# Optimization experiments

Hardware: AMD Instinct MI355X
Metric: run time of the kernel (lower is better)

The kernel has to match this reference:

```python
import jax, jax.numpy as jnp
import numpy as np

B, N_PEP, N_REC, EMB, OUT = 4, 4096, 10, 256, 256


def setup_inputs() -> dict:
    key = jax.random.key(0)
    ks = jax.random.split(key, 9)
    s_emb = 1.0 / np.sqrt(EMB)
    s_2emb = 1.0 / np.sqrt(2 * EMB)
    return {
        "rec_node_feat": jax.random.normal(ks[0], (B, N_PEP, N_REC, EMB), jnp.float32),
        "pep_node_feat": jax.random.normal(ks[1], (B, N_PEP, EMB), jnp.float32),
        "edge_feat": jax.random.normal(ks[2], (B, N_PEP, N_REC, EMB), jnp.float32),
        "Wp_w": jax.random.uniform(ks[3], (OUT, EMB), jnp.float32, -s_emb, s_emb),
        "Wp_b": jax.random.uniform(ks[4], (OUT,), jnp.float32, -s_emb, s_emb),
        "Wr_w": jax.random.uniform(ks[5], (OUT, 2 * EMB), jnp.float32, -s_2emb, s_2emb),
        "Wr_b": jax.random.uniform(ks[6], (OUT,), jnp.float32, -s_2emb, s_2emb),
        "Wv_w": jax.random.uniform(ks[7], (OUT, 2 * EMB), jnp.float32, -s_2emb, s_2emb),
        "Wv_b": jax.random.uniform(ks[8], (OUT,), jnp.float32, -s_2emb, s_2emb),
    }


def reference(rec_node_feat, pep_node_feat, edge_feat,
              Wp_w, Wp_b, Wr_w, Wr_b, Wv_w, Wv_b):
    # pep query: [B, N_pep, out]
    pep_query = jnp.einsum('bnd,od->bno', pep_node_feat, Wp_w) + Wp_b
    # receptor + edge concat: [B, N_pep, 10, 2*emb]
    rec_edge = jnp.concatenate((rec_node_feat, edge_feat), axis=3)
    value = jnp.einsum('bnrd,od->bnro', rec_edge, Wv_w) + Wv_b  # [B,N,10,out]
    key_ = jnp.einsum('bnrd,od->bnro', rec_edge, Wr_w) + Wr_b   # [B,N,10,out]
    scale = 1.0 / np.sqrt(OUT).astype(np.float32)
    # elementwise QK dot over out dim -> [B, N, 10]
    logits = jnp.einsum('bno,bnro->bnr', pep_query, key_) * scale
    attention = jax.nn.softmax(logits, axis=2)  # softmax over 10 neighbors
    # weighted value sum + residual projection
    out = pep_query + jnp.einsum('bnr,bnro->bno', attention, value)
    return out
```

## Files before the change

kernel.cpp:

```cpp
#include <hip/hip_runtime.h>
#include <hip/hip_bf16.h>

#define N_TOK   16384
#define NREC    10
#define EMB     256
#define TWO_EMB 512
#define OUTD    256
#define T_BLK   16
#define THREADS 512

typedef __bf16 bf16x8 __attribute__((ext_vector_type(8)));
typedef float  f32x4  __attribute__((ext_vector_type(4)));

static __device__ __forceinline__ unsigned int f2bf_bits(float f) {
    unsigned int u = __builtin_bit_cast(unsigned int, f);
    u = (u + 0x7fffu + ((u >> 16) & 1u)) >> 16;
    return u & 0xffffu;
}
static __device__ __forceinline__ unsigned int pack2(float a, float b) {
    return f2bf_bits(a) | (f2bf_bits(b) << 16);
}
static __device__ __forceinline__ float bflo(unsigned int u) {
    return __builtin_bit_cast(float, u << 16);
}
static __device__ __forceinline__ float bfhi(unsigned int u) {
    return __builtin_bit_cast(float, u & 0xffff0000u);
}

__global__ void prep_wfrag(const float* __restrict__ Wp,
                           const float* __restrict__ Wr,
                           const float* __restrict__ Wv,
                           short* __restrict__ wp_frag,
                           short* __restrict__ wr_frag,
                           short* __restrict__ wv_frag) {
    int idx = blockIdx.x * blockDim.x + threadIdx.x;
    if (idx < 16 * 8 * 64 * 8) {
        int j = idx & 7, lane = (idx >> 3) & 63, kt = (idx >> 9) & 7, nt = idx >> 12;
        int n = nt * 16 + (lane & 15), k = kt * 32 + ((lane >> 4) << 3) + j;
        wp_frag[idx] = (short)f2bf_bits(Wp[n * EMB + k]);
    }
    if (idx < 32 * 8 * 64 * 8) {
        int j = idx & 7, lane = (idx >> 3) & 63, kt = (idx >> 9) & 7, nt = idx >> 12;
        int n = nt * 16 + (lane & 15), k = kt * 32 + ((lane >> 4) << 3) + j;
        wr_frag[idx] = (short)f2bf_bits(Wr[k * TWO_EMB + n]);
    }
    if (idx < 16 * 16 * 64 * 8) {
        int j = idx & 7, lane = (idx >> 3) & 63, kt = (idx >> 9) & 15, nt = idx >> 13;
        int n = nt * 16 + (lane & 15), k = kt * 32 + ((lane >> 4) << 3) + j;
        wv_frag[idx] = (short)f2bf_bits(Wv[n * TWO_EMB + k]);
    }
}

template<int USE_FRAG>
static __device__ __forceinline__ bf16x8 load_b_rm(const short* __restrict__ frag,
                                                   const float* __restrict__ W,
                                                   int n, int k, int ld) {
    if constexpr (USE_FRAG) {
        return *reinterpret_cast<const bf16x8*>(frag);
    } else {
        const float* s = W + (long)n * ld + k;
        float4 f0 = *reinterpret_cast<const float4*>(s);
        float4 f1 = *reinterpret_cast<const float4*>(s + 4);
        uint4 t = { pack2(f0.x, f0.y), pack2(f0.z, f0.w), pack2(f1.x, f1.y), pack2(f1.z, f1.w) };
        return __builtin_bit_cast(bf16x8, t);
    }
}
template<int USE_FRAG>
static __device__ __forceinline__ bf16x8 load_b_tr(const short* __restrict__ frag,
                                                   const float* __restrict__ W,
                                                   int n, int k, int ld) {
    if constexpr (USE_FRAG) {
        return *reinterpret_cast<const bf16x8*>(frag);
    } else {
        unsigned int p[4];
        #pragma unroll
        for (int jj = 0; jj < 4; ++jj)
            p[jj] = pack2(W[(long)(k + 2 * jj) * ld + n], W[(long)(k + 2 * jj + 1) * ld + n]);
        uint4 t = { p[0], p[1], p[2], p[3] };
        return __builtin_bit_cast(bf16x8, t);
    }
}

static __device__ __forceinline__ void stream_token(
    const float* __restrict__ bp,
    const unsigned char* __restrict__ qrb,
    unsigned char* __restrict__ xz,
    int t, int lane,
    float4 s0l, float4 s0h, float4 s1l, float4 s1h,
    float4 s2l, float4 s2h, float4 s3l, float4 s3h)
{
    uint4 qw = *reinterpret_cast<const uint4*>(qrb + t * 1024 + lane * 16);
    const float qa0 = bflo(qw.x), qa1 = bfhi(qw.x), qa2 = bflo(qw.y), qa3 = bfhi(qw.y);
    const float qa4 = bflo(qw.z), qa5 = bfhi(qw.z), qa6 = bflo(qw.w), qa7 = bfhi(qw.w);
    const float C = 0.0625f * 1.4426950408889634f;

    float s = 0.f;
    float4 xb0 = make_float4(0.f, 0.f, 0.f, 0.f), xb1 = xb0;

    #define LD(r, sl, sh) { sl = *reinterpret_cast<const float4*>(bp + (r) * EMB); \
                            sh = *reinterpret_cast<const float4*>(bp + (r) * EMB + 4); }
    #define PROC(sl, sh) { \
        float p = qa0*(sl).x + qa1*(sl).y + qa2*(sl).z + qa3*(sl).w \
                + qa4*(sh).x + qa5*(sh).y + qa6*(sh).z + qa7*(sh).w; \
        p += __shfl_xor(p, 1); \
        p += __shfl_xor(p, 2); \
        p += __shfl_xor(p, 4); \
        p += __shfl_xor(p, 8); \
        p += __shfl_xor(p, 16); \
        p += __shfl_xor(p, 32); \
        float e = exp2f(p * C);                       \
        s += e; \
        xb0.x += e*(sl).x; xb0.y += e*(sl).y; xb0.z += e*(sl).z; xb0.w += e*(sl).w; \
        xb1.x += e*(sh).x; xb1.y += e*(sh).y; xb1.z += e*(sh).z; xb1.w += e*(sh).w; }

    PROC(s0l, s0h); LD(4, s0l, s0h);
    PROC(s1l, s1h); LD(5, s1l, s1h);
    PROC(s2l, s2h); LD(6, s2l, s2h);
    PROC(s3l, s3h); LD(7, s3l, s3h);
    PROC(s0l, s0h); LD(8, s0l, s0h);
    PROC(s1l, s1h); LD(9, s1l, s1h);
    PROC(s2l, s2h);
    PROC(s3l, s3h);
    PROC(s0l, s0h);
    PROC(s1l, s1h);
    #undef LD
    #undef PROC

    const float inv = 1.f / s;
    uint4 wv4 = { pack2(xb0.x * inv, xb0.y * inv), pack2(xb0.z * inv, xb0.w * inv),
                  pack2(xb1.x * inv, xb1.y * inv), pack2(xb1.z * inv, xb1.w * inv) };
    *reinterpret_cast<uint4*>(xz + 1024 * t + ((lane * 16) ^ ((t & 7) << 4))) = wv4;
}

template<int USE_FRAG>
__launch_bounds__(THREADS, 4)
__global__ void ga5_fused(const float* __restrict__ rec,
                          const float* __restrict__ pep,
                          const float* __restrict__ edge,
                          const float* __restrict__ Wp_w,
                          const float* __restrict__ Wp_b,
                          const float* __restrict__ Wr_w,
                          const float* __restrict__ Wv_w,
                          const float* __restrict__ Wv_b,
                          const short* __restrict__ wp_frag,
                          const short* __restrict__ wr_frag,
                          const short* __restrict__ wv_frag,
                          float* __restrict__ out) {
    __shared__ __align__(16) unsigned char xz[T_BLK * 1024];
    __shared__ __align__(16) unsigned char qbf[T_BLK * 512];
    __shared__ __align__(16) unsigned char qrb[T_BLK * 1024];

    const int tid  = threadIdx.x;
    const int lane = tid & 63;
    const int wave = tid >> 6;
    const int tok0 = blockIdx.x * T_BLK;

    #pragma unroll
    for (int it = 0; it < 2; ++it) {
        int idx = tid + it * THREADS;
        int row = idx >> 6, d4 = (idx & 63) << 2;
        float4 f = *reinterpret_cast<const float4*>(pep + (long)(tok0 + row) * EMB + d4);
        uint2 w = { pack2(f.x, f.y), pack2(f.z, f.w) };
        *reinterpret_cast<uint2*>(xz + 512 * row + ((d4 * 2) ^ ((row & 7) << 4))) = w;
    }
    __syncthreads();

    {
        f32x4 qacc[2] = {};
        #pragma unroll
        for (int kt = 0; kt < 8; ++kt) {
            int kk = kt * 32 + ((lane >> 4) << 3);
            int row = lane & 15;
            bf16x8 a = *reinterpret_cast<const bf16x8*>(xz + 512 * row + ((kk * 2) ^ ((row & 7) << 4)));
            #pragma unroll
            for (int ntl = 0; ntl < 2; ++ntl) {
                int nt = wave * 2 + ntl;
                bf16x8 b = load_b_rm<USE_FRAG>(wp_frag + ((nt * 8 + kt) * 64 + lane) * 8,
                                               Wp_w, nt * 16 + (lane & 15), kk, EMB);
                qacc[ntl] = __builtin_amdgcn_mfma_f32_16x16x32_bf16(a, b, qacc[ntl], 0, 0, 0);
            }
        }
        #pragma unroll
        for (int ntl = 0; ntl < 2; ++ntl) {
            int n = (wave * 2 + ntl) * 16 + (lane & 15);
            float bias = Wp_b[n];
            #pragma unroll
            for (int i = 0; i < 4; ++i) {
                int row = ((lane >> 4) << 2) + i;
                float v = qacc[ntl][i] + bias;
                *reinterpret_cast<unsigned short*>(qbf + 512 * row + ((n * 2) ^ ((row & 7) << 4)))
                    = (unsigned short)f2bf_bits(v);
            }
        }
    }

    const float* srcA = (lane < 32) ? rec : edge;
    const int dloc = (lane * 8) & 255;
    const float* baseA = srcA + (long)(tok0 + wave * 2) * NREC * EMB + dloc;
    const float* baseB = baseA + (long)NREC * EMB;
    float4 a0l = *reinterpret_cast<const float4*>(baseA + 0 * EMB);
    float4 a0h = *reinterpret_cast<const float4*>(baseA + 0 * EMB + 4);
    float4 a1l = *reinterpret_cast<const float4*>(baseA + 1 * EMB);
    float4 a1h = *reinterpret_cast<const float4*>(baseA + 1 * EMB + 4);
    float4 a2l = *reinterpret_cast<const float4*>(baseA + 2 * EMB);
    float4 a2h = *reinterpret_cast<const float4*>(baseA + 2 * EMB + 4);
    float4 a3l = *reinterpret_cast<const float4*>(baseA + 3 * EMB);
    float4 a3h = *reinterpret_cast<const float4*>(baseA + 3 * EMB + 4);
    __syncthreads();

    {
        f32x4 racc[4] = {};
        #pragma unroll
        for (int kt = 0; kt < 8; ++kt) {
            int kk = kt * 32 + ((lane >> 4) << 3);
            int row = lane & 15;
            bf16x8 a = *reinterpret_cast<const bf16x8*>(qbf + 512 * row + ((kk * 2) ^ ((row & 7) << 4)));
            #pragma unroll
            for (int ntl = 0; ntl < 4; ++ntl) {
                int nt = wave * 4 + ntl;
                bf16x8 b = load_b_tr<USE_FRAG>(wr_frag + ((nt * 8 + kt) * 64 + lane) * 8,
                                               Wr_w, nt * 16 + (lane & 15), kk, TWO_EMB);
                racc[ntl] = __builtin_amdgcn_mfma_f32_16x16x32_bf16(a, b, racc[ntl], 0, 0, 0);
            }
        }
        #pragma unroll
        for (int ntl = 0; ntl < 4; ++ntl) {
            int n = (wave * 4 + ntl) * 16 + (lane & 15);
            #pragma unroll
            for (int i = 0; i < 4; ++i) {
                int row = ((lane >> 4) << 2) + i;
                *reinterpret_cast<unsigned short*>(qrb + row * 1024 + n * 2)
                    = (unsigned short)f2bf_bits(racc[ntl][i]);
            }
        }
    }
    __syncthreads();

    stream_token(baseA, qrb, xz, wave * 2, lane, a0l, a0h, a1l, a1h, a2l, a2h, a3l, a3h);
    {
        float4 b0l = *reinterpret_cast<const float4*>(baseB + 0 * EMB);
        float4 b0h = *reinterpret_cast<const float4*>(baseB + 0 * EMB + 4);
        float4 b1l = *reinterpret_cast<const float4*>(baseB + 1 * EMB);
        float4 b1h = *reinterpret_cast<const float4*>(baseB + 1 * EMB + 4);
        float4 b2l = *reinterpret_cast<const float4*>(baseB + 2 * EMB);
        float4 b2h = *reinterpret_cast<const float4*>(baseB + 2 * EMB + 4);
        float4 b3l = *reinterpret_cast<const float4*>(baseB + 3 * EMB);
        float4 b3h = *reinterpret_cast<const float4*>(baseB + 3 * EMB + 4);
        stream_token(baseB, qrb, xz, wave * 2 + 1, lane, b0l, b0h, b1l, b1h, b2l, b2h, b3l, b3h);
    }
    __syncthreads();

    {
        f32x4 oacc[2] = {};
        #pragma unroll
        for (int kt = 0; kt < 16; ++kt) {
            int kk = kt * 32 + ((lane >> 4) << 3);
            int row = lane & 15;
            bf16x8 a = *reinterpret_cast<const bf16x8*>(xz + 1024 * row + ((kk * 2) ^ ((row & 7) << 4)));
            #pragma unroll
            for (int ntl = 0; ntl < 2; ++ntl) {
                int nt = wave * 2 + ntl;
                bf16x8 b = load_b_rm<USE_FRAG>(wv_frag + ((nt * 16 + kt) * 64 + lane) * 8,
                                               Wv_w, nt * 16 + (lane & 15), kk, TWO_EMB);
                oacc[ntl] = __builtin_amdgcn_mfma_f32_16x16x32_bf16(a, b, oacc[ntl], 0, 0, 0);
            }
        }
        #pragma unroll
        for (int ntl = 0; ntl < 2; ++ntl) {
            int n = (wave * 2 + ntl) * 16 + (lane & 15);
            float bv = Wv_b[n];
            #pragma unroll
            for (int i = 0; i < 4; ++i) {
                int row = ((lane >> 4) << 2) + i;
                unsigned short qu = *reinterpret_cast<const unsigned short*>(
                    qbf + 512 * row + ((n * 2) ^ ((row & 7) << 4)));
                float qv = __builtin_bit_cast(float, (unsigned int)qu << 16);
                out[(long)(tok0 + row) * OUTD + n] = qv + oacc[ntl][i] + bv;
            }
        }
    }
}

extern "C" void kernel_launch(void* const* d_in, const int* in_sizes, int n_in,
                              void* d_out, int out_size, void* d_ws, size_t ws_size,
                              hipStream_t stream) {
    const float* rec  = (const float*)d_in[0];
    const float* pep  = (const float*)d_in[1];
    const float* edge = (const float*)d_in[2];
    const float* Wp_w = (const float*)d_in[3];
    const float* Wp_b = (const float*)d_in[4];
    const float* Wr_w = (const float*)d_in[5];
    const float* Wv_w = (const float*)d_in[7];
    const float* Wv_b = (const float*)d_in[8];
    float* out = (float*)d_out;

    const size_t wp_elems = 16 * 8 * 64 * 8;
    const size_t wr_elems = 32 * 8 * 64 * 8;
    const size_t wv_elems = 16 * 16 * 64 * 8;
    const size_t need = (wp_elems + wr_elems + wv_elems) * sizeof(short);
    short* wp_frag = (short*)d_ws;
    short* wr_frag = wp_frag + wp_elems;
    short* wv_frag = wr_frag + wr_elems;

    if (ws_size >= need) {
        prep_wfrag<<<512, 256, 0, stream>>>(Wp_w, Wr_w, Wv_w, wp_frag, wr_frag, wv_frag);
        ga5_fused<1><<<N_TOK / T_BLK, THREADS, 0, stream>>>(rec, pep, edge, Wp_w, Wp_b, Wr_w,
                                                            Wv_w, Wv_b, wp_frag, wr_frag, wv_frag, out);
    } else {
        ga5_fused<0><<<N_TOK / T_BLK, THREADS, 0, stream>>>(rec, pep, edge, Wp_w, Wp_b, Wr_w,
                                                            Wv_w, Wv_b, wp_frag, wr_frag, wv_frag, out);
    }
}
```

Baseline: 97.53 us.

## Split fused kernel into query, streaming and output-projection kernels

Splits the single fused kernel into three launches. The first computes the bf16 query and the query-key projection and writes them to workspace and the output buffer. The second streams rec/edge with one wave per token, computing softmax and the weighted sum into the output buffer as scratch. The third runs the Wv GEMM and adds the residual. The goal is to decouple the memory-bound streaming phase from the GEMM phases so occupancy is higher, and the cross-lane reduction moves to DPP. The cost is extra launches and global round trips for intermediates, plus in-place reuse of the output buffer.

Result: slower. 152.0 us (+55.8%).

```diff
diff --git a/kernel.cpp b/kernel.cpp
--- a/kernel.cpp
+++ b/kernel.cpp
@@ -6,8 +6,6 @@
 #define EMB     256
 #define TWO_EMB 512
 #define OUTD    256
-#define T_BLK   16
-#define THREADS 512
 
 typedef __bf16 bf16x8 __attribute__((ext_vector_type(8)));
 typedef float  f32x4  __attribute__((ext_vector_type(4)));
@@ -25,6 +23,24 @@
 }
 static __device__ __forceinline__ float bfhi(unsigned int u) {
     return __builtin_bit_cast(float, u & 0xffff0000u);
+}
+static __device__ __forceinline__ bf16x8 pack8(float4 f0, float4 f1) {
+    uint4 t = { pack2(f0.x, f0.y), pack2(f0.z, f0.w), pack2(f1.x, f1.y), pack2(f1.z, f1.w) };
+    return __builtin_bit_cast(bf16x8, t);
+}
+
+static __device__ __forceinline__ float wave_sum(float p) {
+    p += __builtin_bit_cast(float, __builtin_amdgcn_update_dpp(
+             0, __builtin_bit_cast(int, p), 0x121, 0xf, 0xf, true));
+    p += __builtin_bit_cast(float, __builtin_amdgcn_update_dpp(
+             0, __builtin_bit_cast(int, p), 0x122, 0xf, 0xf, true));
+    p += __builtin_bit_cast(float, __builtin_amdgcn_update_dpp(
+             0, __builtin_bit_cast(int, p), 0x124, 0xf, 0xf, true));
+    p += __builtin_bit_cast(float, __builtin_amdgcn_update_dpp(
+             0, __builtin_bit_cast(int, p), 0x128, 0xf, 0xf, true));
+    p += __shfl_xor(p, 16);
+    p += __shfl_xor(p, 32);
+    return p;
 }
 
 __global__ void prep_wfrag(const float* __restrict__ Wp,
@@ -59,10 +75,8 @@
         return *reinterpret_cast<const bf16x8*>(frag);
     } else {
         const float* s = W + (long)n * ld + k;
-        float4 f0 = *reinterpret_cast<const float4*>(s);
-        float4 f1 = *reinterpret_cast<const float4*>(s + 4);
-        uint4 t = { pack2(f0.x, f0.y), pack2(f0.z, f0.w), pack2(f1.x, f1.y), pack2(f1.z, f1.w) };
-        return __builtin_bit_cast(bf16x8, t);
+        return pack8(*reinterpret_cast<const float4*>(s),
+                     *reinterpret_cast<const float4*>(s + 4));
     }
 }
 template<int USE_FRAG>
@@ -81,18 +95,109 @@
     }
 }
 
-static __device__ __forceinline__ void stream_token(
-    const float* __restrict__ bp,
-    const unsigned char* __restrict__ qrb,
-    unsigned char* __restrict__ xz,
-    int t, int lane,
-    float4 s0l, float4 s0h, float4 s1l, float4 s1h,
-    float4 s2l, float4 s2h, float4 s3l, float4 s3h)
-{
-    uint4 qw = *reinterpret_cast<const uint4*>(qrb + t * 1024 + lane * 16);
+template<int USE_FRAG>
+__launch_bounds__(256, 4)
+__global__ void ga_qr(const float* __restrict__ pep,
+                      const float* __restrict__ Wp_w,
+                      const float* __restrict__ Wp_b,
+                      const float* __restrict__ Wr_w,
+                      const short* __restrict__ wp_frag,
+                      const short* __restrict__ wr_frag,
+                      unsigned short* __restrict__ qws,
+                      unsigned short* __restrict__ qrws) {
+    __shared__ __align__(16) unsigned char qbf[16 * 512];
+
+    const int tid  = threadIdx.x;
+    const int lane = tid & 63;
+    const int wave = tid >> 6;
+    const int tok0 = blockIdx.x * 16;
+
+    #pragma unroll
+    for (int pass = 0; pass < 2; ++pass) {
+        f32x4 qacc[2] = {};
+        #pragma unroll
+        for (int kt = 0; kt < 8; ++kt) {
+            int kk = kt * 32 + ((lane >> 4) << 3);
+            int row = lane & 15;
+            const float* s = pep + (long)(tok0 + row) * EMB + kk;
+            bf16x8 a = pack8(*reinterpret_cast<const float4*>(s),
+                             *reinterpret_cast<const float4*>(s + 4));
+            #pragma unroll
+            for (int ntl = 0; ntl < 2; ++ntl) {
+                int nt = wave * 4 + pass * 2 + ntl;
+                bf16x8 b = load_b_rm<USE_FRAG>(wp_frag + ((nt * 8 + kt) * 64 + lane) * 8,
+                                               Wp_w, nt * 16 + (lane & 15), kk, EMB);
+                qacc[ntl] = __builtin_amdgcn_mfma_f32_16x16x32_bf16(a, b, qacc[ntl], 0, 0, 0);
+            }
+        }
+        #pragma unroll
+        for (int ntl = 0; ntl < 2; ++ntl) {
+            int n = (wave * 4 + pass * 2 + ntl) * 16 + (lane & 15);
+            float bias = Wp_b[n];
+            #pragma unroll
+            for (int i = 0; i < 4; ++i) {
+                int row = ((lane >> 4) << 2) + i;
+                unsigned short u = (unsigned short)f2bf_bits(qacc[ntl][i] + bias);
+                *reinterpret_cast<unsigned short*>(qbf + 512 * row + ((n * 2) ^ ((row & 7) << 4))) = u;
+                qws[(long)(tok0 + row) * OUTD + n] = u;
+            }
+        }
+    }
+    __syncthreads();
+
+    #pragma unroll
+    for (int pass = 0; pass < 4; ++pass) {
+        f32x4 racc[2] = {};
+        #pragma unroll
+        for (int kt = 0; kt < 8; ++kt) {
+            int kk = kt * 32 + ((lane >> 4) << 3);
+            int row = lane & 15;
+            bf16x8 a = *reinterpret_cast<const bf16x8*>(qbf + 512 * row + ((kk * 2) ^ ((row & 7) << 4)));
+            #pragma unroll
+            for (int ntl = 0; ntl < 2; ++ntl) {
+                int nt = wave * 8 + pass * 2 + ntl;
+                bf16x8 b = load_b_tr<USE_FRAG>(wr_frag + ((nt * 8 + kt) * 64 + lane) * 8,
+                                               Wr_w, nt * 16 + (lane & 15), kk, TWO_EMB);
+                racc[ntl] = __builtin_amdgcn_mfma_f32_16x16x32_bf16(a, b, racc[ntl], 0, 0, 0);
+            }
+        }
+        #pragma unroll
+        for (int ntl = 0; ntl < 2; ++ntl) {
+            int n = (wave * 8 + pass * 2 + ntl) * 16 + (lane & 15);
+            #pragma unroll
+            for (int i = 0; i < 4; ++i) {
+                int row = ((lane >> 4) << 2) + i;
+                qrws[(long)(tok0 + row) * TWO_EMB + n] = (unsigned short)f2bf_bits(racc[ntl][i]);
+            }
+        }
+    }
+}
+
+__launch_bounds__(256, 8)
+__global__ void ga_stream(const float* __restrict__ rec,
+                          const float* __restrict__ edge,
+                          unsigned short* qr_xbar) {
+    const int lane = threadIdx.x & 63;
+    const int wave = threadIdx.x >> 6;
+    const int t = blockIdx.x * 4 + wave;
+
+    const float* srcA = (lane < 32) ? rec : edge;
+    const int dloc = (lane * 8) & 255;
+    const float* bp = srcA + (long)t * NREC * EMB + dloc;
+
+    uint4 qw = *reinterpret_cast<const uint4*>(qr_xbar + (long)t * TWO_EMB + lane * 8);
     const float qa0 = bflo(qw.x), qa1 = bfhi(qw.x), qa2 = bflo(qw.y), qa3 = bfhi(qw.y);
     const float qa4 = bflo(qw.z), qa5 = bfhi(qw.z), qa6 = bflo(qw.w), qa7 = bfhi(qw.w);
-    const float C = 0.0625f * 1.4426950408889634f;
+    const float Cc = 0.0625f * 1.4426950408889634f;
+
+    float4 s0l = *reinterpret_cast<const float4*>(bp + 0 * EMB);
+    float4 s0h = *reinterpret_cast<const float4*>(bp + 0 * EMB + 4);
+    float4 s1l = *reinterpret_cast<const float4*>(bp + 1 * EMB);
+    float4 s1h = *reinterpret_cast<const float4*>(bp + 1 * EMB + 4);
+    float4 s2l = *reinterpret_cast<const float4*>(bp + 2 * EMB);
+    float4 s2h = *reinterpret_cast<const float4*>(bp + 2 * EMB + 4);
+    float4 s3l = *reinterpret_cast<const float4*>(bp + 3 * EMB);
+    float4 s3h = *reinterpret_cast<const float4*>(bp + 3 * EMB + 4);
 
     float s = 0.f;
     float4 xb0 = make_float4(0.f, 0.f, 0.f, 0.f), xb1 = xb0;
@@ -102,13 +207,8 @@
     #define PROC(sl, sh) { \
         float p = qa0*(sl).x + qa1*(sl).y + qa2*(sl).z + qa3*(sl).w \
                 + qa4*(sh).x + qa5*(sh).y + qa6*(sh).z + qa7*(sh).w; \
-        p += __shfl_xor(p, 1); \
-        p += __shfl_xor(p, 2); \
-        p += __shfl_xor(p, 4); \
-        p += __shfl_xor(p, 8); \
-        p += __shfl_xor(p, 16); \
-        p += __shfl_xor(p, 32); \
-        float e = exp2f(p * C);                       \
+        p = wave_sum(p); \
+        float e = exp2f(p * Cc);                      \
         s += e; \
         xb0.x += e*(sl).x; xb0.y += e*(sl).y; xb0.z += e*(sl).z; xb0.w += e*(sl).w; \
         xb1.x += e*(sh).x; xb1.y += e*(sh).y; xb1.z += e*(sh).z; xb1.w += e*(sh).w; }
@@ -129,35 +229,114 @@
     const float inv = 1.f / s;
     uint4 wv4 = { pack2(xb0.x * inv, xb0.y * inv), pack2(xb0.z * inv, xb0.w * inv),
                   pack2(xb1.x * inv, xb1.y * inv), pack2(xb1.z * inv, xb1.w * inv) };
-    *reinterpret_cast<uint4*>(xz + 1024 * t + ((lane * 16) ^ ((t & 7) << 4))) = wv4;
+    *reinterpret_cast<uint4*>(qr_xbar + (long)t * TWO_EMB + lane * 8) = wv4;
 }
 
 template<int USE_FRAG>
-__launch_bounds__(THREADS, 4)
-__global__ void ga5_fused(const float* __restrict__ rec,
-                          const float* __restrict__ pep,
-                          const float* __restrict__ edge,
-                          const float* __restrict__ Wp_w,
-                          const float* __restrict__ Wp_b,
-                          const float* __restrict__ Wr_w,
-                          const float* __restrict__ Wv_w,
-                          const float* __restrict__ Wv_b,
-                          const short* __restrict__ wp_frag,
-                          const short* __restrict__ wr_frag,
-                          const short* __restrict__ wv_frag,
-                          float* __restrict__ out) {
-    __shared__ __align__(16) unsigned char xz[T_BLK * 1024];
-    __shared__ __align__(16) unsigned char qbf[T_BLK * 512];
-    __shared__ __align__(16) unsigned char qrb[T_BLK * 1024];
+__launch_bounds__(256, 4)
+__global__ void ga_out(void* dout,
+                       const unsigned short* __restrict__ qws,
+                       const float* __restrict__ Wv_w,
+                       const float* __restrict__ Wv_b,
+                       const short* __restrict__ wv_frag) {
+    const unsigned short* xbar = (const unsigned short*)dout;
+    float* out = (float*)dout;
 
     const int tid  = threadIdx.x;
     const int lane = tid & 63;
     const int wave = tid >> 6;
-    const int tok0 = blockIdx.x * T_BLK;
+    const int tok0 = blockIdx.x * 16;
+
+    f32x4 oacc[4] = {};
+    #pragma unroll
+    for (int kt = 0; kt < 16; ++kt) {
+        int kk = kt * 32 + ((lane >> 4) << 3);
+        int row = lane & 15;
+        bf16x8 a = *reinterpret_cast<const bf16x8*>(xbar + (long)(tok0 + row) * TWO_EMB + kk);
+        #pragma unroll
+        for (int ntl = 0; ntl < 4; ++ntl) {
+            int nt = wave * 4 + ntl;
+            bf16x8 b = load_b_rm<USE_FRAG>(wv_frag + ((nt * 16 + kt) * 64 + lane) * 8,
+                                           Wv_w, nt * 16 + (lane & 15), kk, TWO_EMB);
+            oacc[ntl] = __builtin_amdgcn_mfma_f32_16x16x32_bf16(a, b, oacc[ntl], 0, 0, 0);
+        }
+    }
+    __syncthreads();
+
+    #pragma unroll
+    for (int ntl = 0; ntl < 4; ++ntl) {
+        int n = (wave * 4 + ntl) * 16 + (lane & 15);
+        float bv = Wv_b[n];
+        #pragma unroll
+        for (int i = 0; i < 4; ++i) {
+            int row = ((lane >> 4) << 2) + i;
+            float qv = bflo((unsigned int)qws[(long)(tok0 + row) * OUTD + n]);
+            out[(long)(tok0 + row) * OUTD + n] = qv + oacc[ntl][i] + bv;
+        }
+    }
+}
+
+static __device__ __forceinline__ void stream_token_f(
+    const float* __restrict__ bp, const unsigned char* __restrict__ qrb,
+    unsigned char* __restrict__ xz, int t, int lane,
+    float4 s0l, float4 s0h, float4 s1l, float4 s1h,
+    float4 s2l, float4 s2h, float4 s3l, float4 s3h)
+{
+    uint4 qw = *reinterpret_cast<const uint4*>(qrb + t * 1024 + lane * 16);
+    const float qa0 = bflo(qw.x), qa1 = bfhi(qw.x), qa2 = bflo(qw.y), qa3 = bfhi(qw.y);
+    const float qa4 = bflo(qw.z), qa5 = bfhi(qw.z), qa6 = bflo(qw.w), qa7 = bfhi(qw.w);
+    const float Cc = 0.0625f * 1.4426950408889634f;
+    float s = 0.f;
+    float4 xb0 = make_float4(0.f, 0.f, 0.f, 0.f), xb1 = xb0;
+    #define LD(r, sl, sh) { sl = *reinterpret_cast<const float4*>(bp + (r) * EMB); \
+                            sh = *reinterpret_cast<const float4*>(bp + (r) * EMB + 4); }
+    #define PROC(sl, sh) { \
+        float p = qa0*(sl).x + qa1*(sl).y + qa2*(sl).z + qa3*(sl).w \
+                + qa4*(sh).x + qa5*(sh).y + qa6*(sh).z + qa7*(sh).w; \
+        p = wave_sum(p); \
+        float e = exp2f(p * Cc); \
+        s += e; \
+        xb0.x += e*(sl).x; xb0.y += e*(sl).y; xb0.z += e*(sl).z; xb0.w += e*(sl).w; \
+        xb1.x += e*(sh).x; xb1.y += e*(sh).y; xb1.z += e*(sh).z; xb1.w += e*(sh).w; }
+    PROC(s0l, s0h); LD(4, s0l, s0h);
+    PROC(s1l, s1h); LD(5, s1l, s1h);
+    PROC(s2l, s2h); LD(6, s2l, s2h);
+    PROC(s3l, s3h); LD(7, s3l, s3h);
+    PROC(s0l, s0h); LD(8, s0l, s0h);
+    PROC(s1l, s1h); LD(9, s1l, s1h);
+    PROC(s2l, s2h);
+    PROC(s3l, s3h);
+    PROC(s0l, s0h);
+    PROC(s1l, s1h);
+    #undef LD
+    #undef PROC
+    const float inv = 1.f / s;
+    uint4 wv4 = { pack2(xb0.x * inv, xb0.y * inv), pack2(xb0.z * inv, xb0.w * inv),
+                  pack2(xb1.x * inv, xb1.y * inv), pack2(xb1.z * inv, xb1.w * inv) };
+    *reinterpret_cast<uint4*>(xz + 1024 * t + ((lane * 16) ^ ((t & 7) << 4))) = wv4;
+}
+
+__launch_bounds__(512, 4)
+__global__ void ga_fallback(const float* __restrict__ rec,
+                            const float* __restrict__ pep,
+                            const float* __restrict__ edge,
+                            const float* __restrict__ Wp_w,
+                            const float* __restrict__ Wp_b,
+                            const float* __restrict__ Wr_w,
+                            const float* __restrict__ Wv_w,
+                            const float* __restrict__ Wv_b,
+                            float* __restrict__ out) {
+    __shared__ __align__(16) unsigned char xz[16 * 1024];
+    __shared__ __align__(16) unsigned char qbf[16 * 512];
+    __shared__ __align__(16) unsigned char qrb[16 * 1024];
+    const int tid  = threadIdx.x;
+    const int lane = tid & 63;
+    const int wave = tid >> 6;
+    const int tok0 = blockIdx.x * 16;
 
     #pragma unroll
     for (int it = 0; it < 2; ++it) {
-        int idx = tid + it * THREADS;
+        int idx = tid + it * 512;
         int row = idx >> 6, d4 = (idx & 63) << 2;
         float4 f = *reinterpret_cast<const float4*>(pep + (long)(tok0 + row) * EMB + d4);
         uint2 w = { pack2(f.x, f.y), pack2(f.z, f.w) };
@@ -175,8 +354,7 @@
             #pragma unroll
             for (int ntl = 0; ntl < 2; ++ntl) {
                 int nt = wave * 2 + ntl;
-                bf16x8 b = load_b_rm<USE_FRAG>(wp_frag + ((nt * 8 + kt) * 64 + lane) * 8,
-                                               Wp_w, nt * 16 + (lane & 15), kk, EMB);
+                bf16x8 b = load_b_rm<0>(nullptr, Wp_w, nt * 16 + (lane & 15), kk, EMB);
                 qacc[ntl] = __builtin_amdgcn_mfma_f32_16x16x32_bf16(a, b, qacc[ntl], 0, 0, 0);
             }
         }
@@ -187,9 +365,8 @@
             #pragma unroll
             for (int i = 0; i < 4; ++i) {
                 int row = ((lane >> 4) << 2) + i;
-                float v = qacc[ntl][i] + bias;
                 *reinterpret_cast<unsigned short*>(qbf + 512 * row + ((n * 2) ^ ((row & 7) << 4)))
-                    = (unsigned short)f2bf_bits(v);
+                    = (unsigned short)f2bf_bits(qacc[ntl][i] + bias);
             }
         }
     }
@@ -208,7 +385,8 @@
     float4 a3h = *reinterpret_cast<const float4*>(baseA + 3 * EMB + 4);
     __syncthreads();
 
-    {
+    #pragma unroll
+    for (int pass = 0; pass < 1; ++pass) {
         f32x4 racc[4] = {};
         #pragma unroll
         for (int kt = 0; kt < 8; ++kt) {
@@ -218,8 +396,7 @@
             #pragma unroll
             for (int ntl = 0; ntl < 4; ++ntl) {
                 int nt = wave * 4 + ntl;
-                bf16x8 b = load_b_tr<USE_FRAG>(wr_frag + ((nt * 8 + kt) * 64 + lane) * 8,
-                                               Wr_w, nt * 16 + (lane & 15), kk, TWO_EMB);
+                bf16x8 b = load_b_tr<0>(nullptr, Wr_w, nt * 16 + (lane & 15), kk, TWO_EMB);
                 racc[ntl] = __builtin_amdgcn_mfma_f32_16x16x32_bf16(a, b, racc[ntl], 0, 0, 0);
             }
         }
@@ -236,7 +413,7 @@
     }
     __syncthreads();
 
-    stream_token(baseA, qrb, xz, wave * 2, lane, a0l, a0h, a1l, a1h, a2l, a2h, a3l, a3h);
+    stream_token_f(baseA, qrb, xz, wave * 2, lane, a0l, a0h, a1l, a1h, a2l, a2h, a3l, a3h);
     {
         float4 b0l = *reinterpret_cast<const float4*>(baseB + 0 * EMB);
         float4 b0h = *reinterpret_cast<const float4*>(baseB + 0 * EMB + 4);
@@ -246,11 +423,12 @@
         float4 b2h = *reinterpret_cast<const float4*>(baseB + 2 * EMB + 4);
         float4 b3l = *reinterpret_cast<const float4*>(baseB + 3 * EMB);
         float4 b3h = *reinterpret_cast<const float4*>(baseB + 3 * EMB + 4);
-        stream_token(baseB, qrb, xz, wave * 2 + 1, lane, b0l, b0h, b1l, b1h, b2l, b2h, b3l, b3h);
-    }
-    __syncthreads();
-
-    {
+        stream_token_f(baseB, qrb, xz, wave * 2 + 1, lane, b0l, b0h, b1l, b1h, b2l, b2h, b3l, b3h);
+    }
+    __syncthreads();
+
+    #pragma unroll
+    for (int pass = 0; pass < 2; ++pass) {
         f32x4 oacc[2] = {};
         #pragma unroll
         for (int kt = 0; kt < 16; ++kt) {
@@ -259,23 +437,21 @@
             bf16x8 a = *reinterpret_cast<const bf16x8*>(xz + 1024 * row + ((kk * 2) ^ ((row & 7) << 4)));
             #pragma unroll
             for (int ntl = 0; ntl < 2; ++ntl) {
-                int nt = wave * 2 + ntl;
-                bf16x8 b = load_b_rm<USE_FRAG>(wv_frag + ((nt * 16 + kt) * 64 + lane) * 8,
-                                               Wv_w, nt * 16 + (lane & 15), kk, TWO_EMB);
+                int nt = wave * 2 + pass + ntl * 2;
+                bf16x8 b = load_b_rm<0>(nullptr, Wv_w, nt * 16 + (lane & 15), kk, TWO_EMB);
                 oacc[ntl] = __builtin_amdgcn_mfma_f32_16x16x32_bf16(a, b, oacc[ntl], 0, 0, 0);
             }
         }
         #pragma unroll
         for (int ntl = 0; ntl < 2; ++ntl) {
-            int n = (wave * 2 + ntl) * 16 + (lane & 15);
+            int n = (wave * 2 + pass + ntl * 2) * 16 + (lane & 15);
             float bv = Wv_b[n];
             #pragma unroll
             for (int i = 0; i < 4; ++i) {
                 int row = ((lane >> 4) << 2) + i;
                 unsigned short qu = *reinterpret_cast<const unsigned short*>(
                     qbf + 512 * row + ((n * 2) ^ ((row & 7) << 4)));
-                float qv = __builtin_bit_cast(float, (unsigned int)qu << 16);
-                out[(long)(tok0 + row) * OUTD + n] = qv + oacc[ntl][i] + bv;
+                out[(long)(tok0 + row) * OUTD + n] = bflo((unsigned int)qu) + oacc[ntl][i] + bv;
             }
         }
     }
@@ -292,22 +468,27 @@
     const float* Wr_w = (const float*)d_in[5];
     const float* Wv_w = (const float*)d_in[7];
     const float* Wv_b = (const float*)d_in[8];
-    float* out = (float*)d_out;
 
     const size_t wp_elems = 16 * 8 * 64 * 8;
     const size_t wr_elems = 32 * 8 * 64 * 8;
     const size_t wv_elems = 16 * 16 * 64 * 8;
-    const size_t need = (wp_elems + wr_elems + wv_elems) * sizeof(short);
+    const size_t frag_bytes = (wp_elems + wr_elems + wv_elems) * sizeof(short);
+    const size_t q_bytes = (size_t)N_TOK * OUTD * sizeof(unsigned short);
+    const size_t need = frag_bytes + q_bytes;
+
     short* wp_frag = (short*)d_ws;
     short* wr_frag = wp_frag + wp_elems;
     short* wv_frag = wr_frag + wr_elems;
+    unsigned short* qws = (unsigned short*)((char*)d_ws + frag_bytes);
 
     if (ws_size >= need) {
         prep_wfrag<<<512, 256, 0, stream>>>(Wp_w, Wr_w, Wv_w, wp_frag, wr_frag, wv_frag);
-        ga5_fused<1><<<N_TOK / T_BLK, THREADS, 0, stream>>>(rec, pep, edge, Wp_w, Wp_b, Wr_w,
-                                                            Wv_w, Wv_b, wp_frag, wr_frag, wv_frag, out);
+        ga_qr<1><<<N_TOK / 16, 256, 0, stream>>>(pep, Wp_w, Wp_b, Wr_w, wp_frag, wr_frag,
+                                                 qws, (unsigned short*)d_out);
+        ga_stream<<<N_TOK / 4, 256, 0, stream>>>(rec, edge, (unsigned short*)d_out);
+        ga_out<1><<<N_TOK / 16, 256, 0, stream>>>(d_out, qws, Wv_w, Wv_b, wv_frag);
     } else {
-        ga5_fused<0><<<N_TOK / T_BLK, THREADS, 0, stream>>>(rec, pep, edge, Wp_w, Wp_b, Wr_w,
-                                                            Wv_w, Wv_b, wp_frag, wr_frag, wv_frag, out);
-    }
-}
+        ga_fallback<<<N_TOK / 16, 512, 0, stream>>>(rec, pep, edge, Wp_w, Wp_b, Wr_w,
+                                                    Wv_w, Wv_b, (float*)d_out);
+    }
+}
```
